# Performance work log

Measured on AMD Instinct MI355X. Metric: run time of the kernel, lower is better.

Reference implementation:

```python
import jax, jax.numpy as jnp
import numpy as np

# Config (Llama-8B-like decode)
B = 64                 # decode batch size
BLOCKS_PER_SEQ = 32    # 4096-token context / 128 block_size
NB = B * BLOCKS_PER_SEQ  # 2048 fetched blocks
NUM_BLOCKS = 2048      # blocks in KV cache
BLOCK_SIZE = 128
KV_HEADS = 8
Q_HEADS = 32
HEAD = 128
CONST_VAL = 10.0                      # VLLM_SOFTMAX_CONST_VAL default
EPS = 1.1754943508222875e-38          # torch.finfo(bfloat16).tiny
SCALE = 1.0 / np.sqrt(HEAD)
NEG = -30000.0                        # mask value for padded slots


def setup_inputs() -> dict:
    key = jax.random.key(0)
    k0, k1, k2, k3 = jax.random.split(key, 4)
    query = jax.random.normal(k0, (B, 1, Q_HEADS * HEAD), dtype=jnp.float32)
    key_cache = jax.random.normal(k1, (NUM_BLOCKS, BLOCK_SIZE, KV_HEADS, HEAD), dtype=jnp.float32)
    value_cache = jax.random.normal(k2, (NUM_BLOCKS, BLOCK_SIZE, KV_HEADS, HEAD), dtype=jnp.float32)
    # each fetched block points at a distinct cache block
    block_list = jax.random.permutation(k3, NUM_BLOCKS)[:NB].astype(jnp.int32)
    # block i belongs to sequence i // BLOCKS_PER_SEQ
    block_groups = jnp.repeat(jnp.arange(B, dtype=jnp.int32), BLOCKS_PER_SEQ)
    block_mapping = jax.nn.one_hot(block_groups, B, dtype=jnp.float32)  # [NB, B]
    # last block of each sequence is half-filled -> masked tail
    pos = jnp.arange(BLOCK_SIZE)
    is_last = (jnp.arange(NB) % BLOCKS_PER_SEQ) == (BLOCKS_PER_SEQ - 1)
    block_bias = jnp.where(is_last[:, None] & (pos[None, :] >= BLOCK_SIZE // 2), NEG, 0.0).astype(jnp.float32)
    return {"query": query, "key_cache": key_cache, "value_cache": value_cache,
            "block_list": block_list, "block_mapping": block_mapping,
            "block_bias": block_bias, "block_groups": block_groups}


def _batch2block(x, block_mapping):
    # ops.batch2block: block_mapping @ x.flatten(1)
    nb = block_mapping.shape[0]
    return (block_mapping @ x.reshape(x.shape[0], -1)).reshape((nb,) + x.shape[1:])


def _block2batch(x, block_mapping):
    # ops.block2batch: block_mapping.T @ x.flatten(1)
    b = block_mapping.shape[1]
    return (block_mapping.T @ x.reshape(x.shape[0], -1)).reshape((b,) + x.shape[1:])


def reference(query, key_cache, value_cache, block_list, block_mapping, block_bias, block_groups):
    # flat_pa with const_norm (pa) softmax normalization, GQA branch
    nb = block_list.shape[0]
    b = block_mapping.shape[1]
    kv_heads, head = key_cache.shape[2], key_cache.shape[3]
    hidden = query.shape[-1]
    q_heads = hidden // head
    qpk = q_heads // kv_heads
    scale = 1.0 / jnp.sqrt(jnp.asarray(head, dtype=query.dtype))

    # scatter queries to their blocks: [NB, kv, qpk, head]
    q = _batch2block(scale * query, block_mapping).reshape(nb, kv_heads, qpk, head)
    # gather KV blocks: [NB, kv, block_size, head]
    k = jnp.transpose(jnp.take(key_cache, block_list, axis=0), (0, 2, 1, 3))
    v = jnp.transpose(jnp.take(value_cache, block_list, axis=0), (0, 2, 1, 3))

    # scores per block: [NB, kv, qpk, block_size]
    attn = jnp.einsum('nkqd,nksd->nkqs', q, k) + block_bias[:, None, None, :]
    # const-normalized exp (attn.sub_(const_val).exp_())
    attn = jnp.exp(attn - CONST_VAL)
    block_sum = attn.sum(axis=-1, keepdims=True)  # [NB, kv, qpk, 1]
    # sum of block sums within each sequence, broadcast back to blocks
    group_sums = _batch2block(_block2batch(block_sum, block_mapping), block_mapping) + EPS
    group_sums = jnp.maximum(block_sum, group_sums)
    attn = attn / group_sums
    out = jnp.einsum('nkqs,nksd->nkqd', attn, v)  # [NB, kv, qpk, head]
    out = _block2batch(out, block_mapping)        # [B, kv, qpk, head]
    return out.reshape(b, q_heads, head)
```

## Files before the change

### kernel.cpp

```cpp
#include <hip/hip_runtime.h>
#include <math.h>

#define KV_HEADS 8
#define Q_HEADS 32
#define HEAD 128
#define BLOCK_SIZE 128
#define CONST_VAL 10.0f
#define F32_TINY 1.1754943508222875e-38f

__global__ __launch_bounds__(256)
void flat_pa_stream(const float* __restrict__ query,
                    const float* __restrict__ key_cache,
                    const float* __restrict__ value_cache,
                    const int*   __restrict__ block_list,
                    const float* __restrict__ block_bias,
                    float*       __restrict__ ws_acc,
                    float*       __restrict__ ws_sum,
                    int B, int blocks_per_seq, int split)
{
    const int g    = blockIdx.x & 1;
    const int sp   = blockIdx.x >> 1;
    const int b    = blockIdx.y;
    const int tid  = threadIdx.x;
    const int wave = tid >> 6;
    const int lane = tid & 63;
    const int half = lane >> 5;
    const int l32  = lane & 31;
    const int dbase = 4 * l32;
    const int kh   = g * 4 + wave;

    const float scale = 0.08838834764831845f;

    float4 qf[4];
    const float* qrow = query + (size_t)b * (Q_HEADS * HEAD)
                              + (size_t)kh * 4 * HEAD + dbase;
    #pragma unroll
    for (int j = 0; j < 4; ++j) {
        float4 t = *reinterpret_cast<const float4*>(qrow + j * HEAD);
        qf[j] = make_float4(t.x * scale, t.y * scale, t.z * scale, t.w * scale);
    }

    float acc[4][4];
    #pragma unroll
    for (int j = 0; j < 4; ++j)
        #pragma unroll
        for (int c = 0; c < 4; ++c) acc[j][c] = 0.f;
    float psum[4] = {0.f, 0.f, 0.f, 0.f};

    const int per = (blocks_per_seq + split - 1) / split;
    const int i0  = sp * per;
    const int i1  = min(i0 + per, blocks_per_seq);
    const int nb0 = b * blocks_per_seq;
    const int khoff = kh * HEAD;

    for (int i = i0; i < i1; ++i) {
        const int n = nb0 + i;
        const long long blk = block_list[n];
        const float* kbase = key_cache   + blk * (long long)(BLOCK_SIZE * KV_HEADS * HEAD) + khoff;
        const float* vbase = value_cache + blk * (long long)(BLOCK_SIZE * KV_HEADS * HEAD) + khoff;
        const float* bias  = block_bias + (long long)n * BLOCK_SIZE;

        #pragma unroll 2
        for (int it = 0; it < BLOCK_SIZE / 2; ++it) {
            const int s = 2 * it + half;
            const size_t roff = (size_t)s * (KV_HEADS * HEAD) + dbase;
            const float4 kv4 = *reinterpret_cast<const float4*>(kbase + roff);
            const float4 vv4 = *reinterpret_cast<const float4*>(vbase + roff);
            const float  bs  = bias[s];

            float part[4];
            #pragma unroll
            for (int j = 0; j < 4; ++j)
                part[j] = qf[j].x * kv4.x + qf[j].y * kv4.y
                        + qf[j].z * kv4.z + qf[j].w * kv4.w;

            #pragma unroll
            for (int m = 1; m <= 16; m <<= 1) {
                #pragma unroll
                for (int j = 0; j < 4; ++j)
                    part[j] += __shfl_xor(part[j], m, 64);
            }

            #pragma unroll
            for (int j = 0; j < 4; ++j) {
                const float p = __expf(part[j] + bs - CONST_VAL);
                psum[j]   += p;
                acc[j][0] += p * vv4.x;
                acc[j][1] += p * vv4.y;
                acc[j][2] += p * vv4.z;
                acc[j][3] += p * vv4.w;
            }
        }
    }

    #pragma unroll
    for (int j = 0; j < 4; ++j) {
        #pragma unroll
        for (int c = 0; c < 4; ++c)
            acc[j][c] += __shfl_xor(acc[j][c], 32, 64);
        psum[j] += __shfl_xor(psum[j], 32, 64);
    }

    const size_t slot = (size_t)(b * split + sp) * 2 + g;
    float* wa = ws_acc + slot * (4 * 4 * HEAD) + (size_t)wave * (4 * HEAD);
    const int j0 = half * 2;
    #pragma unroll
    for (int t = 0; t < 2; ++t) {
        const int j = j0 + t;
        *reinterpret_cast<float4*>(wa + j * HEAD + dbase) =
            make_float4(acc[j][0], acc[j][1], acc[j][2], acc[j][3]);
    }
    if (l32 == 0) {
        ws_sum[slot * 16 + wave * 4 + j0]     = psum[j0];
        ws_sum[slot * 16 + wave * 4 + j0 + 1] = psum[j0 + 1];
    }
}

__global__ __launch_bounds__(256)
void flat_pa_reduce2(const float* __restrict__ ws_acc,
                     const float* __restrict__ ws_sum,
                     float*       __restrict__ out,
                     int B, int split)
{
    const int kh  = blockIdx.x;
    const int b   = blockIdx.y;
    const int tid = threadIdx.x;
    const int g   = kh >> 2;
    const int w   = kh & 3;

    for (int o = tid; o < 4 * HEAD; o += 256) {
        const int j = o >> 7;
        const int d = o & 127;
        float a = 0.f, s = 0.f;
        for (int sp = 0; sp < split; ++sp) {
            const size_t slot = (size_t)(b * split + sp) * 2 + g;
            a += ws_acc[slot * (4 * 4 * HEAD) + (size_t)w * (4 * HEAD) + o];
            s += ws_sum[slot * 16 + w * 4 + j];
        }
        s += F32_TINY;
        out[(size_t)b * (Q_HEADS * HEAD) + (size_t)(kh * 4 + j) * HEAD + d] = a / s;
    }
}

__global__ __launch_bounds__(256)
void flat_pa_single(const float* __restrict__ query,
                    const float* __restrict__ key_cache,
                    const float* __restrict__ value_cache,
                    const int*   __restrict__ block_list,
                    const float* __restrict__ block_bias,
                    float*       __restrict__ out,
                    int blocks_per_seq)
{
    const int kh   = blockIdx.x;
    const int b    = blockIdx.y;
    const int tid  = threadIdx.x;
    const int wave = tid >> 6;
    const int lane = tid & 63;
    const int half = lane >> 5;
    const int l32  = lane & 31;
    const int dbase = 4 * l32;

    const float scale = 0.08838834764831845f;

    float4 qf[4];
    const float* qrow = query + (size_t)b * (Q_HEADS * HEAD)
                              + (size_t)kh * 4 * HEAD + dbase;
    #pragma unroll
    for (int j = 0; j < 4; ++j) {
        float4 t = *reinterpret_cast<const float4*>(qrow + j * HEAD);
        qf[j] = make_float4(t.x * scale, t.y * scale, t.z * scale, t.w * scale);
    }

    float acc[4][4];
    #pragma unroll
    for (int j = 0; j < 4; ++j)
        #pragma unroll
        for (int c = 0; c < 4; ++c) acc[j][c] = 0.f;
    float psum[4] = {0.f, 0.f, 0.f, 0.f};

    const int nb0 = b * blocks_per_seq;
    for (int i = 0; i < blocks_per_seq; ++i) {
        const int n = nb0 + i;
        const long long blk = block_list[n];
        const float* kbase = key_cache   + blk * (long long)(BLOCK_SIZE * KV_HEADS * HEAD) + kh * HEAD;
        const float* vbase = value_cache + blk * (long long)(BLOCK_SIZE * KV_HEADS * HEAD) + kh * HEAD;
        const float* bias  = block_bias + (long long)n * BLOCK_SIZE;

        #pragma unroll 4
        for (int it = 0; it < 16; ++it) {
            const int s = wave * 32 + 2 * it + half;
            const size_t roff = (size_t)s * (KV_HEADS * HEAD) + dbase;
            const float4 kv4 = *reinterpret_cast<const float4*>(kbase + roff);
            const float4 vv4 = *reinterpret_cast<const float4*>(vbase + roff);
            const float  bs  = bias[s];

            float part[4];
            #pragma unroll
            for (int j = 0; j < 4; ++j)
                part[j] = qf[j].x * kv4.x + qf[j].y * kv4.y
                        + qf[j].z * kv4.z + qf[j].w * kv4.w;
            #pragma unroll
            for (int m = 1; m <= 16; m <<= 1) {
                #pragma unroll
                for (int j = 0; j < 4; ++j)
                    part[j] += __shfl_xor(part[j], m, 64);
            }
            #pragma unroll
            for (int j = 0; j < 4; ++j) {
                const float p = __expf(part[j] + bs - CONST_VAL);
                psum[j]   += p;
                acc[j][0] += p * vv4.x;
                acc[j][1] += p * vv4.y;
                acc[j][2] += p * vv4.z;
                acc[j][3] += p * vv4.w;
            }
        }
    }

    #pragma unroll
    for (int j = 0; j < 4; ++j) {
        #pragma unroll
        for (int c = 0; c < 4; ++c)
            acc[j][c] += __shfl_xor(acc[j][c], 32, 64);
        psum[j] += __shfl_xor(psum[j], 32, 64);
    }

    __shared__ float lds_acc[4][4][HEAD];
    __shared__ float lds_sum[4][4];
    if (half == 0) {
        #pragma unroll
        for (int j = 0; j < 4; ++j)
            #pragma unroll
            for (int c = 0; c < 4; ++c)
                lds_acc[wave][j][dbase + c] = acc[j][c];
        if (l32 == 0) {
            #pragma unroll
            for (int j = 0; j < 4; ++j) lds_sum[wave][j] = psum[j];
        }
    }
    __syncthreads();

    for (int o = tid; o < 4 * HEAD; o += 256) {
        const int j = o >> 7;
        const int d = o & 127;
        const float a = lds_acc[0][j][d] + lds_acc[1][j][d]
                      + lds_acc[2][j][d] + lds_acc[3][j][d];
        const float sum = lds_sum[0][j] + lds_sum[1][j]
                        + lds_sum[2][j] + lds_sum[3][j] + F32_TINY;
        out[(size_t)b * (Q_HEADS * HEAD) + (size_t)(kh * 4 + j) * HEAD + d] = a / sum;
    }
}

extern "C" void kernel_launch(void* const* d_in, const int* in_sizes, int n_in,
                              void* d_out, int out_size, void* d_ws, size_t ws_size,
                              hipStream_t stream) {
    const float* query       = (const float*)d_in[0];
    const float* key_cache   = (const float*)d_in[1];
    const float* value_cache = (const float*)d_in[2];
    const int*   block_list  = (const int*)d_in[3];
    const float* block_bias  = (const float*)d_in[5];
    float* out = (float*)d_out;

    const int B  = in_sizes[0] / (Q_HEADS * HEAD);
    const int NB = in_sizes[3];
    const int blocks_per_seq = NB / B;

    int split = (blocks_per_seq + 1) / 2;
    if (split < 1) split = 1;

    const size_t nslots    = (size_t)B * split * 2;
    const size_t acc_elems = nslots * 4 * 4 * HEAD;
    const size_t sum_elems = nslots * 16;
    const size_t need = (acc_elems + sum_elems) * sizeof(float);

    if (ws_size >= need) {
        float* ws_acc = (float*)d_ws;
        float* ws_sum = ws_acc + acc_elems;
        dim3 grid1(2 * split, B);
        flat_pa_stream<<<grid1, 256, 0, stream>>>(
            query, key_cache, value_cache, block_list, block_bias,
            ws_acc, ws_sum, B, blocks_per_seq, split);
        dim3 grid2(KV_HEADS, B);
        flat_pa_reduce2<<<grid2, 256, 0, stream>>>(ws_acc, ws_sum, out, B, split);
    } else {
        dim3 grid(KV_HEADS, B);
        flat_pa_single<<<grid, 256, 0, stream>>>(
            query, key_cache, value_cache, block_list, block_bias, out, blocks_per_seq);
    }
}
```

Before: 407.1 us.

## Use one 512-thread block per KV block covering all eight KV heads

The streaming kernel now launches one 512-thread workgroup per (sequence, fetched block), with each of the 8 waves handling one KV head, instead of two 256-thread groups covering 4 heads each over pairs of blocks. The split now equals blocks_per_seq, so each workgroup processes exactly one cache block, which makes its reads of a block's K/V rows contiguous across heads. The inner loop unroll goes from 2 to 4. The workspace doubles in partial slots, so the reduce kernel does more work and needs more memory, and the larger unroll may raise register pressure.

```diff
diff --git a/kernel.cpp b/kernel.cpp
--- a/kernel.cpp
+++ b/kernel.cpp
@@ -8,26 +8,24 @@
 #define CONST_VAL 10.0f
 #define F32_TINY 1.1754943508222875e-38f
 
-__global__ __launch_bounds__(256)
-void flat_pa_stream(const float* __restrict__ query,
-                    const float* __restrict__ key_cache,
-                    const float* __restrict__ value_cache,
-                    const int*   __restrict__ block_list,
-                    const float* __restrict__ block_bias,
-                    float*       __restrict__ ws_acc,
-                    float*       __restrict__ ws_sum,
-                    int B, int blocks_per_seq, int split)
+__global__ __launch_bounds__(512)
+void flat_pa_stream8(const float* __restrict__ query,
+                     const float* __restrict__ key_cache,
+                     const float* __restrict__ value_cache,
+                     const int*   __restrict__ block_list,
+                     const float* __restrict__ block_bias,
+                     float*       __restrict__ ws_acc,
+                     float*       __restrict__ ws_sum,
+                     int B, int blocks_per_seq, int split)
 {
-    const int g    = blockIdx.x & 1;
-    const int sp   = blockIdx.x >> 1;
+    const int sp   = blockIdx.x;
     const int b    = blockIdx.y;
     const int tid  = threadIdx.x;
-    const int wave = tid >> 6;
+    const int kh   = tid >> 6;
     const int lane = tid & 63;
     const int half = lane >> 5;
     const int l32  = lane & 31;
     const int dbase = 4 * l32;
-    const int kh   = g * 4 + wave;
 
     const float scale = 0.08838834764831845f;
 
@@ -60,7 +58,7 @@
         const float* vbase = value_cache + blk * (long long)(BLOCK_SIZE * KV_HEADS * HEAD) + khoff;
         const float* bias  = block_bias + (long long)n * BLOCK_SIZE;
 
-        #pragma unroll 2
+        #pragma unroll 4
         for (int it = 0; it < BLOCK_SIZE / 2; ++it) {
             const int s = 2 * it + half;
             const size_t roff = (size_t)s * (KV_HEADS * HEAD) + dbase;
@@ -101,8 +99,8 @@
         psum[j] += __shfl_xor(psum[j], 32, 64);
     }
 
-    const size_t slot = (size_t)(b * split + sp) * 2 + g;
-    float* wa = ws_acc + slot * (4 * 4 * HEAD) + (size_t)wave * (4 * HEAD);
+    const size_t slot = (size_t)b * split + sp;
+    float* wa = ws_acc + slot * (KV_HEADS * 4 * HEAD) + (size_t)kh * (4 * HEAD);
     const int j0 = half * 2;
     #pragma unroll
     for (int t = 0; t < 2; ++t) {
@@ -111,13 +109,13 @@
             make_float4(acc[j][0], acc[j][1], acc[j][2], acc[j][3]);
     }
     if (l32 == 0) {
-        ws_sum[slot * 16 + wave * 4 + j0]     = psum[j0];
-        ws_sum[slot * 16 + wave * 4 + j0 + 1] = psum[j0 + 1];
+        ws_sum[slot * (KV_HEADS * 4) + kh * 4 + j0]     = psum[j0];
+        ws_sum[slot * (KV_HEADS * 4) + kh * 4 + j0 + 1] = psum[j0 + 1];
     }
 }
 
 __global__ __launch_bounds__(256)
-void flat_pa_reduce2(const float* __restrict__ ws_acc,
+void flat_pa_reduce8(const float* __restrict__ ws_acc,
                      const float* __restrict__ ws_sum,
                      float*       __restrict__ out,
                      int B, int split)
@@ -125,17 +123,15 @@
     const int kh  = blockIdx.x;
     const int b   = blockIdx.y;
     const int tid = threadIdx.x;
-    const int g   = kh >> 2;
-    const int w   = kh & 3;
 
     for (int o = tid; o < 4 * HEAD; o += 256) {
         const int j = o >> 7;
         const int d = o & 127;
         float a = 0.f, s = 0.f;
         for (int sp = 0; sp < split; ++sp) {
-            const size_t slot = (size_t)(b * split + sp) * 2 + g;
-            a += ws_acc[slot * (4 * 4 * HEAD) + (size_t)w * (4 * HEAD) + o];
-            s += ws_sum[slot * 16 + w * 4 + j];
+            const size_t slot = (size_t)b * split + sp;
+            a += ws_acc[slot * (KV_HEADS * 4 * HEAD) + (size_t)kh * (4 * HEAD) + o];
+            s += ws_sum[slot * (KV_HEADS * 4) + kh * 4 + j];
         }
         s += F32_TINY;
         out[(size_t)b * (Q_HEADS * HEAD) + (size_t)(kh * 4 + j) * HEAD + d] = a / s;
@@ -265,23 +261,23 @@
     const int NB = in_sizes[3];
     const int blocks_per_seq = NB / B;
 
-    int split = (blocks_per_seq + 1) / 2;
+    int split = blocks_per_seq;
     if (split < 1) split = 1;
 
-    const size_t nslots    = (size_t)B * split * 2;
-    const size_t acc_elems = nslots * 4 * 4 * HEAD;
-    const size_t sum_elems = nslots * 16;
+    const size_t nslots    = (size_t)B * split;
+    const size_t acc_elems = nslots * KV_HEADS * 4 * HEAD;
+    const size_t sum_elems = nslots * KV_HEADS * 4;
     const size_t need = (acc_elems + sum_elems) * sizeof(float);
 
     if (ws_size >= need) {
         float* ws_acc = (float*)d_ws;
         float* ws_sum = ws_acc + acc_elems;
-        dim3 grid1(2 * split, B);
-        flat_pa_stream<<<grid1, 256, 0, stream>>>(
+        dim3 grid1(split, B);
+        flat_pa_stream8<<<grid1, 512, 0, stream>>>(
             query, key_cache, value_cache, block_list, block_bias,
             ws_acc, ws_sum, B, blocks_per_seq, split);
         dim3 grid2(KV_HEADS, B);
-        flat_pa_reduce2<<<grid2, 256, 0, stream>>>(ws_acc, ws_sum, out, B, split);
+        flat_pa_reduce8<<<grid2, 256, 0, stream>>>(ws_acc, ws_sum, out, B, split);
     } else {
         dim3 grid(KV_HEADS, B);
         flat_pa_single<<<grid, 256, 0, stream>>>(
```

Result: slower. 529.8 us (+30.1%).
